# Kernel optimization log

Measured on AMD Instinct MI355X. Metric: run time of the kernel, lower is better.

The kernel has to match this reference:

```python
import math
import jax, jax.numpy as jnp
import numpy as np

B, T, C, H = 2, 1024, 1024, 16
D = C // H          # head_dim = 64
ROPE_M = 32         # min(head_dim//2, 64)
FB_M = 32
ROPE_BASE = 10000.0


def setup_inputs() -> dict:
    key = jax.random.key(0)
    ks = jax.random.split(key, 8)
    x = jax.random.normal(ks[0], (B, T, C), dtype=jnp.float32)
    # default coords: per-token position, d_coord=1
    coords = jnp.broadcast_to(jnp.arange(T, dtype=jnp.float32)[None, :, None], (B, T, 1))
    # c_attn / c_proj linear params (torch Linear: y = x @ W.T + b)
    W_attn = jax.random.normal(ks[1], (3 * C, C), dtype=jnp.float32) * (1.0 / math.sqrt(C))
    b_attn = jnp.zeros((3 * C,), dtype=jnp.float32)
    W_proj = jax.random.normal(ks[2], (C, C), dtype=jnp.float32) * (1.0 / math.sqrt(C))
    b_proj = jnp.zeros((C,), dtype=jnp.float32)
    # RoPE freq bank, kind='log': exp(linspace(log(1/base), 0, m)) replicated over d_coord
    steps = jnp.exp(jnp.linspace(math.log(1.0 / ROPE_BASE), 0.0, ROPE_M)).astype(jnp.float32)
    W_rope = steps[:, None]  # [m, d_coord=1]
    # Fourier-bias bank, kind='gaussian', sigma=1.0
    W_fb = jax.random.normal(ks[3], (FB_M, 1), dtype=jnp.float32)
    # betas are zero-init nn.Parameters; use small random values so bias path is exercised
    beta_cos = jax.random.normal(ks[4], (FB_M,), dtype=jnp.float32) * 0.1
    beta_sin = jax.random.normal(ks[5], (FB_M,), dtype=jnp.float32) * 0.1
    return {"x": x, "coords": coords, "W_attn": W_attn, "b_attn": b_attn,
            "W_proj": W_proj, "b_proj": b_proj, "W_rope": W_rope, "W_fb": W_fb,
            "beta_cos": beta_cos, "beta_sin": beta_sin}


def _rope_rotate(z, c, s):
    # z: [B,H,T,D]; c,s: [B,1,T,ROPE_M]; rotates first 2*ROPE_M channels pairwise
    zr = z[..., :2 * ROPE_M].reshape(*z.shape[:-1], ROPE_M, 2)
    y0 = zr[..., 0] * c - zr[..., 1] * s
    y1 = zr[..., 0] * s + zr[..., 1] * c
    y = jnp.stack((y0, y1), axis=-1).reshape(*z.shape[:-1], 2 * ROPE_M)
    return jnp.concatenate([y, z[..., 2 * ROPE_M:]], axis=-1)


def reference(x, coords, W_attn, b_attn, W_proj, b_proj, W_rope, W_fb, beta_cos, beta_sin):
    qkv = x @ W_attn.T + b_attn                      # [B,T,3C]
    q, k, v = jnp.split(qkv, 3, axis=-1)
    to_heads = lambda z: z.reshape(B, T, H, D).transpose(0, 2, 1, 3)  # [B,H,T,D]
    q, k, v = to_heads(q), to_heads(k), to_heads(v)
    # Iron RoPE: theta = coords @ W_rope.T -> [B,T,ROPE_M]
    theta = coords @ W_rope.T
    c = jnp.cos(theta)[:, None]                      # [B,1,T,ROPE_M]
    s = jnp.sin(theta)[:, None]
    q = _rope_rotate(q, c, s)
    k = _rope_rotate(k, c, s)
    att = jnp.einsum('bhqd,bhkd->bhqk', q, k) * (1.0 / math.sqrt(D))
    # relative Fourier bias (shared across heads)
    delta = coords[:, :, None, :] - coords[:, None, :, :]   # [B,Tq,Tk,1]
    S = jnp.einsum('bqkd,md->bqkm', delta, W_fb)            # [B,Tq,Tk,FB_M]
    bias = (jnp.cos(S) * beta_cos + jnp.sin(S) * beta_sin).sum(-1)  # [B,Tq,Tk]
    att = att + (1.0 / math.sqrt(FB_M)) * bias[:, None]     # [B,H,Tq,Tk]
    # non-causal: mask buffer is all ones -> no masking; dropout p=0 -> identity
    att = jax.nn.softmax(att, axis=-1)
    y = jnp.einsum('bhqk,bhkd->bhqd', att, v)
    y = y.transpose(0, 2, 1, 3).reshape(B, T, C)
    y = y @ W_proj.T + b_proj
    return x + y
```

## Files before the change

kernel.cpp:

```cpp
#include <hip/hip_runtime.h>
#include <math.h>

#define Bc 2
#define Tc 1024
#define Cc 1024
#define Hc 16
#define Dc 64
#define DE 128

typedef unsigned short u16;
typedef __attribute__((ext_vector_type(8))) short bf16x8;
typedef __attribute__((ext_vector_type(4))) float f32x4;

#define QSCALE 0.1803368801111243f
#define FIXED_M 24.0f

static __device__ inline u16 f2b(float f) {
    unsigned u = __float_as_uint(f);
    u = (u + 0x7fffu + ((u >> 16) & 1u)) >> 16;
    return (u16)u;
}
static __device__ inline float b2f(u16 h) {
    return __uint_as_float((unsigned)h << 16);
}

typedef __attribute__((address_space(1))) const unsigned int g_u32;
typedef __attribute__((address_space(3))) unsigned int l_u32;
static __device__ __forceinline__ void gll16(const void* g, void* l) {
    __builtin_amdgcn_global_load_lds((g_u32*)g, (l_u32*)l, 16, 0, 0);
}

__global__ __launch_bounds__(256) void cast_all(
    const float* __restrict__ x, const float* __restrict__ wa, const float* __restrict__ wp,
    u16* __restrict__ xb, u16* __restrict__ wab, u16* __restrict__ wpb)
{
    const int NX = Bc * Tc * Cc;
    const int NA = 3 * Cc * Cc;
    int i = (blockIdx.x * 256 + threadIdx.x) * 4;
    const float* src; u16* dst; int off;
    if (i < NX)            { src = x;  dst = xb;  off = i; }
    else if (i < NX + NA)  { src = wa; dst = wab; off = i - NX; }
    else                   { src = wp; dst = wpb; off = i - NX - NA; }
    float4 v = *(const float4*)(src + off);
    ushort4 o;
    o.x = f2b(v.x); o.y = f2b(v.y); o.z = f2b(v.z); o.w = f2b(v.w);
    *(ushort4*)(dst + off) = o;
}

template<int TM, int TN, int WR, int WC, bool OUT_BF16>
__global__ __launch_bounds__(256) void gemm_abt(
    const u16* __restrict__ A, const u16* __restrict__ Bm,
    const float* __restrict__ bias, const float* __restrict__ resid,
    float* __restrict__ outf, u16* __restrict__ outb, int M, int N, int K)
{
    constexpr int WTM = TM / WR;
    constexpr int WTN = TN / WC;
    constexpr int FI = WTM / 16;
    constexpr int FJ = WTN / 16;
    constexpr int ITA = TM / 32;
    constexpr int ITB = TN / 32;
    __shared__ u16 ldsA[2][TM * 64];
    __shared__ u16 ldsB[2][TN * 64];
    const int tid  = threadIdx.x;
    const int wave = tid >> 6;
    const int lane = tid & 63;
    const int l15  = lane & 15;
    const int quad = lane >> 4;
    const int wm = wave / WC;
    const int wn = wave % WC;
    const int tm = blockIdx.y * TM;
    const int tn = blockIdx.x * TN;

    f32x4 acc[FI][FJ] = {};

    auto stage = [&](int buf, int k0) {
#pragma unroll
        for (int it = 0; it < ITA; ++it) {
            int p = it * 256 + tid;
            int row = p >> 3;
            int c = ((p & 7) ^ (row & 7)) * 8;
            gll16(A + (size_t)(tm + row) * K + k0 + c,
                  &ldsA[buf][(it * 256 + (wave << 6)) * 8]);
        }
#pragma unroll
        for (int it = 0; it < ITB; ++it) {
            int p = it * 256 + tid;
            int row = p >> 3;
            int c = ((p & 7) ^ (row & 7)) * 8;
            gll16(Bm + (size_t)(tn + row) * K + k0 + c,
                  &ldsB[buf][(it * 256 + (wave << 6)) * 8]);
        }
    };

    const int NK = K >> 6;
    stage(0, 0);
    for (int ki = 0; ki < NK; ++ki) {
        const int buf = ki & 1;
        __syncthreads();
        if (ki + 1 < NK) stage(buf ^ 1, (ki + 1) << 6);
#pragma unroll
        for (int kk = 0; kk < 2; ++kk) {
            bf16x8 af[FI], bf[FJ];
#pragma unroll
            for (int i = 0; i < FI; ++i) {
                int row = wm * WTM + i * 16 + l15;
                int slot = (kk * 4 + quad) ^ (row & 7);
                af[i] = *(const bf16x8*)&ldsA[buf][row * 64 + slot * 8];
            }
#pragma unroll
            for (int j = 0; j < FJ; ++j) {
                int row = wn * WTN + j * 16 + l15;
                int slot = (kk * 4 + quad) ^ (row & 7);
                bf[j] = *(const bf16x8*)&ldsB[buf][row * 64 + slot * 8];
            }
#pragma unroll
            for (int i = 0; i < FI; ++i)
#pragma unroll
                for (int j = 0; j < FJ; ++j)
                    acc[i][j] = __builtin_amdgcn_mfma_f32_16x16x32_bf16(af[i], bf[j], acc[i][j], 0, 0, 0);
        }
    }

#pragma unroll
    for (int i = 0; i < FI; ++i) {
        int row = tm + wm * WTM + i * 16 + quad * 4;
#pragma unroll
        for (int j = 0; j < FJ; ++j) {
            int col = tn + wn * WTN + j * 16 + l15;
            float bb = bias[col];
#pragma unroll
            for (int r = 0; r < 4; ++r) {
                float v = acc[i][j][r] + bb;
                if (resid) v += resid[(size_t)(row + r) * N + col];
                if (OUT_BF16) outb[(size_t)(row + r) * N + col] = f2b(v);
                else          outf[(size_t)(row + r) * N + col] = v;
            }
        }
    }
}

__global__ __launch_bounds__(256) void prep_kernel(
    const u16* __restrict__ qkv, const float* __restrict__ coords,
    const float* __restrict__ W_rope, const float* __restrict__ W_fb,
    const float* __restrict__ bcos, const float* __restrict__ bsin,
    u16* __restrict__ qe, u16* __restrict__ ke, u16* __restrict__ vt)
{
    const int bt = blockIdx.x;
    const int b = bt >> 10;
    const int t = bt & (Tc - 1);
    const float coord = coords[bt];
    const int tid = threadIdx.x;
    const u16* row = qkv + (size_t)bt * 3072;
    const int e  = tid * 4;
    const int h  = e >> 6;
    const int d0 = e & 63;
    const int m0 = d0 >> 1;

    float th0 = coord * W_rope[m0];
    float th1 = coord * W_rope[m0 + 1];
    float s0 = sinf(th0), c0 = cosf(th0);
    float s1 = sinf(th1), c1 = cosf(th1);

    float q0 = b2f(row[e]), q1 = b2f(row[e + 1]), q2 = b2f(row[e + 2]), q3 = b2f(row[e + 3]);
    float k0 = b2f(row[1024 + e]), k1 = b2f(row[1025 + e]), k2 = b2f(row[1026 + e]), k3 = b2f(row[1027 + e]);
    float v0 = b2f(row[2048 + e]), v1 = b2f(row[2049 + e]), v2 = b2f(row[2050 + e]), v3 = b2f(row[2051 + e]);

    size_t qb = ((size_t)(b * Hc + h) * Tc + t) * DE + d0;
    qe[qb + 0] = f2b((q0 * c0 - q1 * s0) * QSCALE);
    qe[qb + 1] = f2b((q0 * s0 + q1 * c0) * QSCALE);
    qe[qb + 2] = f2b((q2 * c1 - q3 * s1) * QSCALE);
    qe[qb + 3] = f2b((q2 * s1 + q3 * c1) * QSCALE);
    ke[qb + 0] = f2b(k0 * c0 - k1 * s0);
    ke[qb + 1] = f2b(k0 * s0 + k1 * c0);
    ke[qb + 2] = f2b(k2 * c1 - k3 * s1);
    ke[qb + 3] = f2b(k2 * s1 + k3 * c1);

    size_t vb = ((size_t)(b * Hc + h) * Dc + d0) * Tc + t;
    vt[vb]          = f2b(v0);
    vt[vb + Tc]     = f2b(v1);
    vt[vb + 2 * Tc] = f2b(v2);
    vt[vb + 3 * Tc] = f2b(v3);

    {
        const int hh = tid >> 4;
        const int s  = tid & 15;
        const int m  = 2 * s;
        float thf0 = coord * W_fb[m],     thf1 = coord * W_fb[m + 1];
        float sn0 = sinf(thf0), cn0 = cosf(thf0);
        float sn1 = sinf(thf1), cn1 = cosf(thf1);
        float bc0 = bcos[m], bs0 = bsin[m], bc1 = bcos[m + 1], bs1 = bsin[m + 1];
        const float SC = 1.41421356237f * QSCALE;
        unsigned u1 = (unsigned)f2b((bc0 * cn0 + bs0 * sn0) * SC) |
                      ((unsigned)f2b((bc1 * cn1 + bs1 * sn1) * SC) << 16);
        unsigned u2 = (unsigned)f2b((bc0 * sn0 - bs0 * cn0) * SC) |
                      ((unsigned)f2b((bc1 * sn1 - bs1 * cn1) * SC) << 16);
        unsigned cp = (unsigned)f2b(cn0) | ((unsigned)f2b(cn1) << 16);
        unsigned sp = (unsigned)f2b(sn0) | ((unsigned)f2b(sn1) << 16);
        size_t base = ((size_t)(b * Hc + hh) * Tc + t) * DE + 64;
        *(unsigned*)&qe[base + m]      = u1;
        *(unsigned*)&qe[base + 32 + m] = u2;
        *(unsigned*)&ke[base + m]      = cp;
        *(unsigned*)&ke[base + 32 + m] = sp;
    }
}

__global__ __launch_bounds__(256) void attn_kernel(
    const u16* __restrict__ qe, const u16* __restrict__ ke,
    const u16* __restrict__ vt, u16* __restrict__ yb)
{
    __shared__ u16 ldsK[2][64 * 128];
    __shared__ u16 ldsV[2][64 * 64];
    __shared__ u16 plds[4][16][72];
    const int tid  = threadIdx.x;
    const int wave = tid >> 6;
    const int lane = tid & 63;
    const int l15  = lane & 15;
    const int quad = lane >> 4;
    const int qt = blockIdx.x * 64;
    const int h  = blockIdx.y;
    const int b  = blockIdx.z;

    const u16* Q  = qe + ((size_t)(b * Hc + h) * Tc) * DE;
    const u16* Kp = ke + ((size_t)(b * Hc + h) * Tc) * DE;
    const u16* Vp = vt + ((size_t)(b * Hc + h) * Dc) * Tc;

    bf16x8 qf[4];
    {
        const u16* qrow = Q + (size_t)(qt + wave * 16 + l15) * DE + quad * 8;
#pragma unroll
        for (int c = 0; c < 4; ++c) qf[c] = *(const bf16x8*)(qrow + c * 32);
    }

    auto stageKV = [&](int buf, int kt) {
#pragma unroll
        for (int it = 0; it < 4; ++it) {
            int p = it * 256 + tid;
            int row = p >> 4;
            int c = (p & 15) ^ (row & 15);
            gll16(Kp + (size_t)(kt + row) * DE + c * 8,
                  &ldsK[buf][(it * 256 + (wave << 6)) * 8]);
        }
#pragma unroll
        for (int it = 0; it < 2; ++it) {
            int p = it * 256 + tid;
            int row = p >> 3;
            int c = (p & 7) ^ (row & 7);
            gll16(Vp + (size_t)row * Tc + kt + c * 8,
                  &ldsV[buf][(it * 256 + (wave << 6)) * 8]);
        }
    };

    f32x4 o[4] = {};
    float lrow[4] = {0.f, 0.f, 0.f, 0.f};

    stageKV(0, 0);
    for (int ki = 0; ki < Tc / 64; ++ki) {
        const int buf = ki & 1;
        __syncthreads();
        if (ki + 1 < Tc / 64) stageKV(buf ^ 1, (ki + 1) * 64);

        f32x4 sf[4] = {};
#pragma unroll
        for (int f = 0; f < 4; ++f) {
#pragma unroll
            for (int c = 0; c < 4; ++c) {
                int row = f * 16 + l15;
                int slot = (c * 4 + quad) ^ (row & 15);
                bf16x8 kf = *(const bf16x8*)&ldsK[buf][row * 128 + slot * 8];
                sf[f] = __builtin_amdgcn_mfma_f32_16x16x32_bf16(qf[c], kf, sf[f], 0, 0, 0);
            }
        }
        float psum[4] = {0.f, 0.f, 0.f, 0.f};
#pragma unroll
        for (int f = 0; f < 4; ++f)
#pragma unroll
            for (int r = 0; r < 4; ++r) {
                float p = __builtin_amdgcn_exp2f(sf[f][r] - FIXED_M);
                u16 tp = (u16)(__float_as_uint(p) >> 16);
                plds[wave][quad * 4 + r][f * 16 + l15] = tp;
                psum[r] += b2f(tp);
            }
#pragma unroll
        for (int r = 0; r < 4; ++r) {
            float v = psum[r];
#pragma unroll
            for (int off = 1; off < 16; off <<= 1) v += __shfl_xor(v, off);
            lrow[r] += v;
        }

#pragma unroll
        for (int c = 0; c < 2; ++c) {
            bf16x8 pa = *(const bf16x8*)&plds[wave][l15][c * 32 + quad * 8];
#pragma unroll
            for (int df = 0; df < 4; ++df) {
                int row = df * 16 + l15;
                int slot = (c * 4 + quad) ^ (row & 7);
                bf16x8 vf = *(const bf16x8*)&ldsV[buf][row * 64 + slot * 8];
                o[df] = __builtin_amdgcn_mfma_f32_16x16x32_bf16(pa, vf, o[df], 0, 0, 0);
            }
        }
    }

    float rl[4];
#pragma unroll
    for (int r = 0; r < 4; ++r) rl[r] = 1.0f / lrow[r];
#pragma unroll
    for (int df = 0; df < 4; ++df)
#pragma unroll
        for (int r = 0; r < 4; ++r) {
            int t = qt + wave * 16 + quad * 4 + r;
            int d = df * 16 + l15;
            yb[((size_t)b * Tc + t) * Cc + h * Dc + d] = f2b(o[df][r] * rl[r]);
        }
}

extern "C" void kernel_launch(void* const* d_in, const int* in_sizes, int n_in,
                              void* d_out, int out_size, void* d_ws, size_t ws_size,
                              hipStream_t stream) {
    const float* x      = (const float*)d_in[0];
    const float* coords = (const float*)d_in[1];
    const float* W_attn = (const float*)d_in[2];
    const float* b_attn = (const float*)d_in[3];
    const float* W_proj = (const float*)d_in[4];
    const float* b_proj = (const float*)d_in[5];
    const float* W_rope = (const float*)d_in[6];
    const float* W_fb   = (const float*)d_in[7];
    const float* bcos   = (const float*)d_in[8];
    const float* bsin   = (const float*)d_in[9];
    float* out = (float*)d_out;

    char* w = (char*)d_ws;
    const size_t MB = 1024 * 1024;
    u16* xb     = (u16*)(w + 0);
    u16* wab    = (u16*)(w + 4 * MB);
    u16* wpb    = (u16*)(w + 10 * MB);
    u16* qkvb16 = (u16*)(w + 12 * MB);
    u16* qext   = (u16*)(w + 24 * MB);
    u16* kext   = (u16*)(w + 32 * MB);
    u16* vtw    = (u16*)(w + 40 * MB);
    u16* yb     = (u16*)(w + 44 * MB);

    const int NALL = (Bc * Tc * Cc + 3 * Cc * Cc + Cc * Cc) / 4;
    cast_all<<<NALL / 256, 256, 0, stream>>>(x, W_attn, W_proj, xb, wab, wpb);

    dim3 g1(3 * Cc / 128, Bc * Tc / 64);
    gemm_abt<64, 128, 2, 2, true><<<g1, 256, 0, stream>>>(
        xb, wab, b_attn, nullptr, nullptr, qkvb16, Bc * Tc, 3 * Cc, Cc);

    prep_kernel<<<Bc * Tc, 256, 0, stream>>>(qkvb16, coords, W_rope, W_fb, bcos, bsin, qext, kext, vtw);

    dim3 g2(Tc / 64, Hc, Bc);
    attn_kernel<<<g2, 256, 0, stream>>>(qext, kext, vtw, yb);

    dim3 g3(Cc / 64, Bc * Tc / 64);
    gemm_abt<64, 64, 2, 2, false><<<g3, 256, 0, stream>>>(
        yb, wpb, b_proj, x, out, nullptr, Bc * Tc, Cc, Cc);
}
```

Baseline: 174.7 us.

## Process two query sub-tiles per wave in attention with 128-thread blocks

The attention kernel now uses 2 waves per block instead of 4, and each wave handles 32 query rows (two 16-row MFMA tiles). Each K and V fragment read from LDS is reused across both query sub-tiles, halving LDS reads per MFMA. The per-block row-sum cross-lane shuffle reduction moves out of the key loop and runs once at the end. In exchange each wave needs more registers for its accumulators and Q fragments, and a block has fewer waves to hide latency.

```diff
diff --git a/kernel.cpp b/kernel.cpp
--- a/kernel.cpp
+++ b/kernel.cpp
@@ -204,13 +204,13 @@
     }
 }
 
-__global__ __launch_bounds__(256) void attn_kernel(
+__global__ __launch_bounds__(128) void attn_kernel(
     const u16* __restrict__ qe, const u16* __restrict__ ke,
     const u16* __restrict__ vt, u16* __restrict__ yb)
 {
     __shared__ u16 ldsK[2][64 * 128];
     __shared__ u16 ldsV[2][64 * 64];
-    __shared__ u16 plds[4][16][72];
+    __shared__ u16 plds[2][32][72];
     const int tid  = threadIdx.x;
     const int wave = tid >> 6;
     const int lane = tid & 63;
@@ -224,34 +224,35 @@
     const u16* Kp = ke + ((size_t)(b * Hc + h) * Tc) * DE;
     const u16* Vp = vt + ((size_t)(b * Hc + h) * Dc) * Tc;
 
-    bf16x8 qf[4];
-    {
-        const u16* qrow = Q + (size_t)(qt + wave * 16 + l15) * DE + quad * 8;
-#pragma unroll
-        for (int c = 0; c < 4; ++c) qf[c] = *(const bf16x8*)(qrow + c * 32);
+    bf16x8 qf[2][4];
+#pragma unroll
+    for (int i = 0; i < 2; ++i) {
+        const u16* qrow = Q + (size_t)(qt + wave * 32 + i * 16 + l15) * DE + quad * 8;
+#pragma unroll
+        for (int c = 0; c < 4; ++c) qf[i][c] = *(const bf16x8*)(qrow + c * 32);
     }
 
     auto stageKV = [&](int buf, int kt) {
 #pragma unroll
-        for (int it = 0; it < 4; ++it) {
-            int p = it * 256 + tid;
+        for (int it = 0; it < 8; ++it) {
+            int p = it * 128 + tid;
             int row = p >> 4;
             int c = (p & 15) ^ (row & 15);
             gll16(Kp + (size_t)(kt + row) * DE + c * 8,
-                  &ldsK[buf][(it * 256 + (wave << 6)) * 8]);
-        }
-#pragma unroll
-        for (int it = 0; it < 2; ++it) {
-            int p = it * 256 + tid;
+                  &ldsK[buf][(it * 128 + (wave << 6)) * 8]);
+        }
+#pragma unroll
+        for (int it = 0; it < 4; ++it) {
+            int p = it * 128 + tid;
             int row = p >> 3;
             int c = (p & 7) ^ (row & 7);
             gll16(Vp + (size_t)row * Tc + kt + c * 8,
-                  &ldsV[buf][(it * 256 + (wave << 6)) * 8]);
+                  &ldsV[buf][(it * 128 + (wave << 6)) * 8]);
         }
     };
 
-    f32x4 o[4] = {};
-    float lrow[4] = {0.f, 0.f, 0.f, 0.f};
+    f32x4 o[2][4] = {};
+    float lrow[2][4] = {};
 
     stageKV(0, 0);
     for (int ki = 0; ki < Tc / 64; ++ki) {
@@ -259,7 +260,7 @@
         __syncthreads();
         if (ki + 1 < Tc / 64) stageKV(buf ^ 1, (ki + 1) * 64);
 
-        f32x4 sf[4] = {};
+        f32x4 sf[2][4] = {};
 #pragma unroll
         for (int f = 0; f < 4; ++f) {
 #pragma unroll
@@ -267,51 +268,61 @@
                 int row = f * 16 + l15;
                 int slot = (c * 4 + quad) ^ (row & 15);
                 bf16x8 kf = *(const bf16x8*)&ldsK[buf][row * 128 + slot * 8];
-                sf[f] = __builtin_amdgcn_mfma_f32_16x16x32_bf16(qf[c], kf, sf[f], 0, 0, 0);
-            }
-        }
-        float psum[4] = {0.f, 0.f, 0.f, 0.f};
-#pragma unroll
-        for (int f = 0; f < 4; ++f)
-#pragma unroll
-            for (int r = 0; r < 4; ++r) {
-                float p = __builtin_amdgcn_exp2f(sf[f][r] - FIXED_M);
-                u16 tp = (u16)(__float_as_uint(p) >> 16);
-                plds[wave][quad * 4 + r][f * 16 + l15] = tp;
-                psum[r] += b2f(tp);
-            }
-#pragma unroll
-        for (int r = 0; r < 4; ++r) {
-            float v = psum[r];
-#pragma unroll
-            for (int off = 1; off < 16; off <<= 1) v += __shfl_xor(v, off);
-            lrow[r] += v;
-        }
+#pragma unroll
+                for (int i = 0; i < 2; ++i)
+                    sf[i][f] = __builtin_amdgcn_mfma_f32_16x16x32_bf16(qf[i][c], kf, sf[i][f], 0, 0, 0);
+            }
+        }
+#pragma unroll
+        for (int i = 0; i < 2; ++i)
+#pragma unroll
+            for (int f = 0; f < 4; ++f)
+#pragma unroll
+                for (int r = 0; r < 4; ++r) {
+                    float p = __builtin_amdgcn_exp2f(sf[i][f][r] - FIXED_M);
+                    u16 tp = (u16)(__float_as_uint(p) >> 16);
+                    plds[wave][i * 16 + quad * 4 + r][f * 16 + l15] = tp;
+                    lrow[i][r] += b2f(tp);
+                }
 
 #pragma unroll
         for (int c = 0; c < 2; ++c) {
-            bf16x8 pa = *(const bf16x8*)&plds[wave][l15][c * 32 + quad * 8];
+            bf16x8 pa[2];
+#pragma unroll
+            for (int i = 0; i < 2; ++i)
+                pa[i] = *(const bf16x8*)&plds[wave][i * 16 + l15][c * 32 + quad * 8];
 #pragma unroll
             for (int df = 0; df < 4; ++df) {
                 int row = df * 16 + l15;
                 int slot = (c * 4 + quad) ^ (row & 7);
                 bf16x8 vf = *(const bf16x8*)&ldsV[buf][row * 64 + slot * 8];
-                o[df] = __builtin_amdgcn_mfma_f32_16x16x32_bf16(pa, vf, o[df], 0, 0, 0);
-            }
-        }
-    }
-
-    float rl[4];
-#pragma unroll
-    for (int r = 0; r < 4; ++r) rl[r] = 1.0f / lrow[r];
-#pragma unroll
-    for (int df = 0; df < 4; ++df)
+#pragma unroll
+                for (int i = 0; i < 2; ++i)
+                    o[i][df] = __builtin_amdgcn_mfma_f32_16x16x32_bf16(pa[i], vf, o[i][df], 0, 0, 0);
+            }
+        }
+    }
+
+    float rl[2][4];
+#pragma unroll
+    for (int i = 0; i < 2; ++i)
 #pragma unroll
         for (int r = 0; r < 4; ++r) {
-            int t = qt + wave * 16 + quad * 4 + r;
-            int d = df * 16 + l15;
-            yb[((size_t)b * Tc + t) * Cc + h * Dc + d] = f2b(o[df][r] * rl[r]);
-        }
+            float v = lrow[i][r];
+#pragma unroll
+            for (int off = 1; off < 16; off <<= 1) v += __shfl_xor(v, off);
+            rl[i][r] = 1.0f / v;
+        }
+#pragma unroll
+    for (int i = 0; i < 2; ++i)
+#pragma unroll
+        for (int df = 0; df < 4; ++df)
+#pragma unroll
+            for (int r = 0; r < 4; ++r) {
+                int t = qt + wave * 32 + i * 16 + quad * 4 + r;
+                int d = df * 16 + l15;
+                yb[((size_t)b * Tc + t) * Cc + h * Dc + d] = f2b(o[i][df][r] * rl[i][r]);
+            }
 }
 
 extern "C" void kernel_launch(void* const* d_in, const int* in_sizes, int n_in,
@@ -350,7 +361,7 @@
     prep_kernel<<<Bc * Tc, 256, 0, stream>>>(qkvb16, coords, W_rope, W_fb, bcos, bsin, qext, kext, vtw);
 
     dim3 g2(Tc / 64, Hc, Bc);
-    attn_kernel<<<g2, 256, 0, stream>>>(qext, kext, vtw, yb);
+    attn_kernel<<<g2, 128, 0, stream>>>(qext, kext, vtw, yb);
 
     dim3 g3(Cc / 64, Bc * Tc / 64);
     gemm_abt<64, 64, 2, 2, false><<<g3, 256, 0, stream>>>(
```

Result: no change. 175.2 us (+0.3%).

## Switch attention to 32x32 MFMA with split-K waves and LDS reduction

Applied to the files above, without the earlier changes.

Rewrites the attention inner loop to use 32x32x16 bf16 MFMA tiles. Waves are split into two query halves and two key halves, and the partial outputs and row sums from the two key-half waves are combined through LDS at the end. Row-sum shuffles move out of the loop into the epilogue. The grid is also reordered so heads and batch vary fastest across blocks, which may help K/V cache locality. The cost is more accumulator registers and an extra LDS reduction step.

```diff
diff --git a/kernel.cpp b/kernel.cpp
--- a/kernel.cpp
+++ b/kernel.cpp
@@ -11,6 +11,7 @@
 typedef unsigned short u16;
 typedef __attribute__((ext_vector_type(8))) short bf16x8;
 typedef __attribute__((ext_vector_type(4))) float f32x4;
+typedef __attribute__((ext_vector_type(16))) float f32x16;
 
 #define QSCALE 0.1803368801111243f
 #define FIXED_M 24.0f
@@ -210,25 +211,28 @@
 {
     __shared__ u16 ldsK[2][64 * 128];
     __shared__ u16 ldsV[2][64 * 64];
-    __shared__ u16 plds[4][16][72];
+    __shared__ u16 plds[4][32][40];
+    __shared__ float lM[2][32];
     const int tid  = threadIdx.x;
     const int wave = tid >> 6;
     const int lane = tid & 63;
-    const int l15  = lane & 15;
-    const int quad = lane >> 4;
-    const int qt = blockIdx.x * 64;
-    const int h  = blockIdx.y;
-    const int b  = blockIdx.z;
+    const int l31  = lane & 31;
+    const int half = lane >> 5;
+    const int qw = wave & 1;
+    const int kw = wave >> 1;
+    const int h  = blockIdx.x & 15;
+    const int b  = blockIdx.x >> 4;
+    const int qt = blockIdx.y * 64;
 
     const u16* Q  = qe + ((size_t)(b * Hc + h) * Tc) * DE;
     const u16* Kp = ke + ((size_t)(b * Hc + h) * Tc) * DE;
     const u16* Vp = vt + ((size_t)(b * Hc + h) * Dc) * Tc;
 
-    bf16x8 qf[4];
+    bf16x8 qf[8];
     {
-        const u16* qrow = Q + (size_t)(qt + wave * 16 + l15) * DE + quad * 8;
-#pragma unroll
-        for (int c = 0; c < 4; ++c) qf[c] = *(const bf16x8*)(qrow + c * 32);
+        const u16* qrow = Q + (size_t)(qt + qw * 32 + l31) * DE + half * 8;
+#pragma unroll
+        for (int c = 0; c < 8; ++c) qf[c] = *(const bf16x8*)(qrow + c * 16);
     }
 
     auto stageKV = [&](int buf, int kt) {
@@ -250,8 +254,8 @@
         }
     };
 
-    f32x4 o[4] = {};
-    float lrow[4] = {0.f, 0.f, 0.f, 0.f};
+    f32x16 o[2] = {};
+    float lrow[16] = {};
 
     stageKV(0, 0);
     for (int ki = 0; ki < Tc / 64; ++ki) {
@@ -259,59 +263,71 @@
         __syncthreads();
         if (ki + 1 < Tc / 64) stageKV(buf ^ 1, (ki + 1) * 64);
 
-        f32x4 sf[4] = {};
-#pragma unroll
-        for (int f = 0; f < 4; ++f) {
-#pragma unroll
-            for (int c = 0; c < 4; ++c) {
-                int row = f * 16 + l15;
-                int slot = (c * 4 + quad) ^ (row & 15);
-                bf16x8 kf = *(const bf16x8*)&ldsK[buf][row * 128 + slot * 8];
-                sf[f] = __builtin_amdgcn_mfma_f32_16x16x32_bf16(qf[c], kf, sf[f], 0, 0, 0);
-            }
-        }
-        float psum[4] = {0.f, 0.f, 0.f, 0.f};
-#pragma unroll
-        for (int f = 0; f < 4; ++f)
-#pragma unroll
-            for (int r = 0; r < 4; ++r) {
-                float p = __builtin_amdgcn_exp2f(sf[f][r] - FIXED_M);
-                u16 tp = (u16)(__float_as_uint(p) >> 16);
-                plds[wave][quad * 4 + r][f * 16 + l15] = tp;
-                psum[r] += b2f(tp);
-            }
-#pragma unroll
-        for (int r = 0; r < 4; ++r) {
-            float v = psum[r];
-#pragma unroll
-            for (int off = 1; off < 16; off <<= 1) v += __shfl_xor(v, off);
-            lrow[r] += v;
-        }
-
-#pragma unroll
-        for (int c = 0; c < 2; ++c) {
-            bf16x8 pa = *(const bf16x8*)&plds[wave][l15][c * 32 + quad * 8];
-#pragma unroll
-            for (int df = 0; df < 4; ++df) {
-                int row = df * 16 + l15;
-                int slot = (c * 4 + quad) ^ (row & 7);
-                bf16x8 vf = *(const bf16x8*)&ldsV[buf][row * 64 + slot * 8];
-                o[df] = __builtin_amdgcn_mfma_f32_16x16x32_bf16(pa, vf, o[df], 0, 0, 0);
-            }
-        }
-    }
-
-    float rl[4];
-#pragma unroll
-    for (int r = 0; r < 4; ++r) rl[r] = 1.0f / lrow[r];
-#pragma unroll
-    for (int df = 0; df < 4; ++df)
-#pragma unroll
-        for (int r = 0; r < 4; ++r) {
-            int t = qt + wave * 16 + quad * 4 + r;
-            int d = df * 16 + l15;
-            yb[((size_t)b * Tc + t) * Cc + h * Dc + d] = f2b(o[df][r] * rl[r]);
-        }
+        f32x16 sf = {};
+#pragma unroll
+        for (int c = 0; c < 8; ++c) {
+            int row = kw * 32 + l31;
+            int slot = (c * 2 + half) ^ (row & 15);
+            bf16x8 kf = *(const bf16x8*)&ldsK[buf][row * 128 + slot * 8];
+            sf = __builtin_amdgcn_mfma_f32_32x32x16_bf16(qf[c], kf, sf, 0, 0, 0);
+        }
+#pragma unroll
+        for (int r = 0; r < 16; ++r) {
+            float p = __builtin_amdgcn_exp2f(sf[r] - FIXED_M);
+            u16 tp = (u16)(__float_as_uint(p) >> 16);
+            int row = (r & 3) + 8 * (r >> 2) + 4 * half;
+            plds[wave][row][l31] = tp;
+            lrow[r] += b2f(tp);
+        }
+#pragma unroll
+        for (int kc = 0; kc < 2; ++kc) {
+            bf16x8 pa = *(const bf16x8*)&plds[wave][l31][kc * 16 + half * 8];
+#pragma unroll
+            for (int dt = 0; dt < 2; ++dt) {
+                int vrow = dt * 32 + l31;
+                int chunk = (kw * 32 + kc * 16 + half * 8) >> 3;
+                int slot = chunk ^ (vrow & 7);
+                bf16x8 vf = *(const bf16x8*)&ldsV[buf][vrow * 64 + slot * 8];
+                o[dt] = __builtin_amdgcn_mfma_f32_32x32x16_bf16(pa, vf, o[dt], 0, 0, 0);
+            }
+        }
+    }
+
+    __syncthreads();
+
+#pragma unroll
+    for (int r = 0; r < 16; ++r) {
+        float v = lrow[r];
+#pragma unroll
+        for (int off = 1; off < 32; off <<= 1) v += __shfl_xor(v, off);
+        lrow[r] = v;
+    }
+
+    float* oM = (float*)&ldsK[0][0];
+    if (kw == 1) {
+#pragma unroll
+        for (int r = 0; r < 16; ++r) {
+            int row = (r & 3) + 8 * (r >> 2) + 4 * half;
+#pragma unroll
+            for (int dt = 0; dt < 2; ++dt)
+                oM[(qw * 32 + row) * 64 + dt * 32 + l31] = o[dt][r];
+            if (l31 == 0) lM[qw][row] = lrow[r];
+        }
+    }
+    __syncthreads();
+    if (kw == 0) {
+#pragma unroll
+        for (int r = 0; r < 16; ++r) {
+            int row = (r & 3) + 8 * (r >> 2) + 4 * half;
+            float rl = 1.0f / (lrow[r] + lM[qw][row]);
+            int t = qt + qw * 32 + row;
+#pragma unroll
+            for (int dt = 0; dt < 2; ++dt) {
+                float val = (o[dt][r] + oM[(qw * 32 + row) * 64 + dt * 32 + l31]) * rl;
+                yb[((size_t)b * Tc + t) * Cc + h * Dc + dt * 32 + l31] = f2b(val);
+            }
+        }
+    }
 }
 
 extern "C" void kernel_launch(void* const* d_in, const int* in_sizes, int n_in,
@@ -349,7 +365,7 @@
 
     prep_kernel<<<Bc * Tc, 256, 0, stream>>>(qkvb16, coords, W_rope, W_fb, bcos, bsin, qext, kext, vtw);
 
-    dim3 g2(Tc / 64, Hc, Bc);
+    dim3 g2(Hc * Bc, Tc / 64);
     attn_kernel<<<g2, 256, 0, stream>>>(qext, kext, vtw, yb);
 
     dim3 g3(Cc / 64, Bc * Tc / 64);
```

Result: faster. 169.6 us (-2.9%).
